# Performance work log

Measured on AMD Instinct MI355X. Metric: run time of the kernel, lower is better.

## Reference

```python
import jax, jax.numpy as jnp
import numpy as np

B, T, F, H = 128, 512, 128, 512
ODE_STEPS = 2
MAX_DT = 1.0


def setup_inputs() -> dict:
    key = jax.random.key(0)
    ks = jax.random.split(key, 8)
    xavier = lambda k, shape: jax.random.uniform(
        k, shape, jnp.float32, -1.0, 1.0) * np.sqrt(6.0 / (shape[0] + shape[1]))
    return {
        "x": jax.random.normal(ks[0], (B, T, F), jnp.float32),
        "time_diffs": jax.random.uniform(ks[1], (B, T), jnp.float32),
        "Wz": xavier(ks[2], (H, F + H)), "bz": jnp.zeros((H,), jnp.float32),
        "Wr": xavier(ks[3], (H, F + H)), "br": jnp.zeros((H,), jnp.float32),
        "Wg": xavier(ks[4], (H, F + H)), "bg": jnp.zeros((H,), jnp.float32),
    }


def reference(x, time_diffs, Wz, bz, Wr, br, Wg, bg):
    hidden = Wz.shape[0]

    def ode_func(x_t, h):
        # dh/dt = (1 - z) * (g - h)
        xh = jnp.concatenate([x_t, h], axis=-1)           # [b, F+H]
        z = jax.nn.sigmoid(xh @ Wz.T + bz)
        r = jax.nn.sigmoid(xh @ Wr.T + br)
        g = jnp.tanh(jnp.concatenate([x_t, r * h], axis=-1) @ Wg.T + bg)
        return (1.0 - z) * (g - h)

    def rk4(x_t, h, dt):
        k1 = ode_func(x_t, h)
        k2 = ode_func(x_t, h + 0.5 * dt * k1)
        k3 = ode_func(x_t, h + 0.5 * dt * k2)
        k4 = ode_func(x_t, h + dt * k3)
        return h + (dt / 6.0) * (k1 + 2.0 * k2 + 2.0 * k3 + k4)

    def step(h, inp):
        x_t, td = inp                                     # [b,F], [b]
        dt = (jnp.minimum(td, MAX_DT) / ODE_STEPS)[:, None]
        for _ in range(ODE_STEPS):                        # small fixed count
            h = rk4(x_t, h, dt)
        return h, h

    h0 = jnp.zeros((x.shape[0], hidden), x.dtype)
    _, out = jax.lax.scan(step, h0, (jnp.swapaxes(x, 0, 1), time_diffs.T))
    return jnp.swapaxes(out, 0, 1)                        # [b, T, H]
```

## Files before the change

### kernel.cpp

```cpp
#include <hip/hip_runtime.h>


namespace {
constexpr int kB = 128, kT = 512, kF = 128, kH = 512, kFH = 640;
constexpr int QZ4 = 0, QR4 = 16384, QG4 = 32768;
constexpr int WXZ4 = 49152, WXR4 = 57344, WXG4 = 65536;
constexpr size_t CS_OFF = (size_t)73728 * 16;
constexpr float HSCL = 100.0f;
}

typedef _Float16 h2_t __attribute__((ext_vector_type(2)));

__device__ __forceinline__ unsigned short f2h(float f) {
  return __builtin_bit_cast(unsigned short, (_Float16)f);
}
__device__ __forceinline__ unsigned pack2h(float a, float b) {
  return (unsigned)f2h(a) | ((unsigned)f2h(b) << 16);
}
__device__ __forceinline__ float dot2(unsigned w, unsigned h, float acc) {
  return __builtin_amdgcn_fdot2(__builtin_bit_cast(h2_t, w),
                                __builtin_bit_cast(h2_t, h), acc, false);
}
__device__ __forceinline__ float dot2x4(uint4 w, uint4 h, float acc) {
  acc = dot2(w.x, h.x, acc); acc = dot2(w.y, h.y, acc);
  acc = dot2(w.z, h.z, acc); acc = dot2(w.w, h.w, acc);
  return acc;
}
__device__ __forceinline__ uint4 pk8(const float* s) {
  const float4 a = *(const float4*)s;
  const float4 b = *(const float4*)(s + 4);
  uint4 o;
  o.x = pack2h(a.x, a.y); o.y = pack2h(a.z, a.w);
  o.z = pack2h(b.x, b.y); o.w = pack2h(b.z, b.w);
  return o;
}
__device__ __forceinline__ int sd4(unsigned a, unsigned b, int acc) {
  return __builtin_amdgcn_sdot4((int)a, (int)b, acc, false);
}
__device__ __forceinline__ void dslice(const uint4 w, const unsigned* hq,
                                       int p, int& acc) {
  acc = sd4(w.x, hq[4 * p + 0], acc);
  acc = sd4(w.y, hq[4 * p + 1], acc);
  acc = sd4(w.z, hq[4 * p + 2], acc);
  acc = sd4(w.w, hq[4 * p + 3], acc);
}

#define DECL_OPQ(v, ptr, s)                                          \
  uint4 v = (ptr)[(s) * kH];                                         \
  asm volatile("" : "+v"(v.x), "+v"(v.y), "+v"(v.z), "+v"(v.w))

__global__ void quant_weights(const float* __restrict__ Wz,
                              const float* __restrict__ Wr,
                              const float* __restrict__ Wg,
                              void* __restrict__ ws) {
  const int bx = blockIdx.x;
  const int gate = bx >> 9, j = bx & 511;
  const float* W = (gate == 0) ? Wz : (gate == 1) ? Wr : Wg;
  const float* row = W + (size_t)j * kFH;
  const int lane = threadIdx.x;
  uint4* ws4 = (uint4*)ws;

  const float* src = row + kF + lane * 8;
  float v[8]; float m = 0.f;
#pragma unroll
  for (int i = 0; i < 8; ++i) { v[i] = src[i]; m = fmaxf(m, fabsf(v[i])); }
#pragma unroll
  for (int off = 32; off; off >>= 1) m = fmaxf(m, __shfl_xor(m, off));
  const float inv = 127.f / m;
  unsigned u0 = 0, u1 = 0;
#pragma unroll
  for (int i = 0; i < 4; ++i) {
    int q = __float2int_rn(v[i] * inv); q = max(-127, min(127, q));
    u0 |= ((unsigned)(q & 255)) << (8 * i);
  }
#pragma unroll
  for (int i = 0; i < 4; ++i) {
    int q = __float2int_rn(v[4 + i] * inv); q = max(-127, min(127, q));
    u1 |= ((unsigned)(q & 255)) << (8 * i);
  }
  const int p = lane >> 1, sub = lane & 1;
  const int qbase = (gate == 0) ? QZ4 : (gate == 1) ? QR4 : QG4;
  *(uint2*)((char*)ws + ((size_t)(qbase + p * kH + j)) * 16 + sub * 8) =
      make_uint2(u0, u1);
  if (lane < 16) {
    const int xbase = (gate == 0) ? WXZ4 : (gate == 1) ? WXR4 : WXG4;
    ws4[xbase + lane * kH + j] = pk8(row + lane * 8);
  }
  if (lane == 0)
    ((float*)((char*)ws + CS_OFF))[gate * 512 + j] = m / (127.f * HSCL);
}

__global__ __launch_bounds__(1024, 4) void cgru_i8s(
    const float* __restrict__ x, const float* __restrict__ td,
    const float* __restrict__ bz, const float* __restrict__ br,
    const float* __restrict__ bg, const uint4* __restrict__ ws,
    float* __restrict__ out) {
  __shared__ uint4 WLa[2][6][kH];
  __shared__ uint4 WLg[2][3][kH];
  __shared__ unsigned hq[kH / 4];
  __shared__ unsigned rq[kH / 4];
  __shared__ unsigned xpk[kF / 2];
  __shared__ float gpart[kH];

  const int b = blockIdx.x;
  const int tid = threadIdx.x;
  const int j = tid & (kH - 1);
  const int half = tid >> 9;

  const uint4* __restrict__ wQa = ws + (half ? QR4 : QZ4) + j;
  const uint4* __restrict__ wQg = ws + QG4 + j;
  const uint4* __restrict__ wxa = ws + (half ? WXR4 : WXZ4) + j;
  const uint4* __restrict__ wxg = ws + WXG4 + j;
  const float* cs = (const float*)((const char*)ws + CS_OFF);
  const float csa = cs[(half ? 512 : 0) + j];
  const float csg = cs[1024 + j];

  DECL_OPQ(a0, wQa, 0); DECL_OPQ(a1, wQa, 1); DECL_OPQ(a2, wQa, 2);
  DECL_OPQ(a3, wQa, 3); DECL_OPQ(a4, wQa, 4); DECL_OPQ(a5, wQa, 5);
  DECL_OPQ(a6, wQa, 6); DECL_OPQ(a7, wQa, 7);
  {
    const uint4* qa = ws + (half ? QR4 : QZ4);
#pragma unroll
    for (int q = 0; q < 6; ++q) WLa[half][q][j] = qa[(8 + q) * kH + j];
#pragma unroll
    for (int q = 0; q < 3; ++q)
      WLg[half][q][j] = (ws + QG4)[((half ? 16 : 0) + q) * kH + j];
  }

  const float ba = half ? br[j] : bz[j];
  const float bgv = bg[j];
  float hb = 0.f, hs = 0.f, kacc = 0.f, zv = 0.f, dtv = 0.f;
  if (tid < kH / 4) hq[tid] = 0;

  for (int t = 0; t < kT; ++t) {
    if (tid < kF / 2) {
      const float2 xv =
          *(const float2*)(x + ((size_t)b * kT + t) * kF + 2 * tid);
      xpk[tid] = pack2h(xv.x, xv.y);
    }
    __syncthreads();

    const uint4* xp4 = (const uint4*)xpk;
    float ax = ba;
#pragma unroll 4
    for (int p = 0; p < 16; ++p) ax = dot2x4(wxa[p * kH], xp4[p], ax);
    float agx = half ? 0.f : bgv;
#pragma unroll 4
    for (int p = 0; p < 8; ++p)
      agx = dot2x4(wxg[(half * 8 + p) * kH], xp4[half * 8 + p], agx);
    if (half == 0) dtv = fminf(td[(size_t)b * kT + t], 1.0f) * 0.5f;

    for (int e = 0; e < 8; ++e) {
      const int s = e & 3;
      int ah = 0;
      dslice(a0, hq, 0, ah); dslice(a1, hq, 1, ah);
      dslice(a2, hq, 2, ah); dslice(a3, hq, 3, ah);
      dslice(a4, hq, 4, ah); dslice(a5, hq, 5, ah);
      dslice(a6, hq, 6, ah); dslice(a7, hq, 7, ah);
#pragma unroll
      for (int q = 0; q < 6; ++q)
        dslice(WLa[half][q][j], hq, 8 + q, ah);
#pragma unroll 6
      for (int p = 14; p < 32; ++p)
        dslice(wQa[p * kH], hq, p, ah);
      const float aA = ax + csa * (float)ah;

      if (half == 0) {
        zv = 1.0f / (1.0f + __expf(-aA));
      } else {
        const float r = 1.0f / (1.0f + __expf(-aA));
        const float hv = (float)((const char*)hq)[j] * (1.0f / HSCL);
        int q = __float2int_rn(fminf(fmaxf(r * hv, -1.27f), 1.27f) * HSCL);
        ((char*)rq)[j] = (char)q;
      }
      __syncthreads();

      int gh = 0;
      const int bs = half << 4;
#pragma unroll
      for (int q = 0; q < 3; ++q)
        dslice(WLg[half][q][j], rq, bs + q, gh);
#pragma unroll 4
      for (int p = bs + 3; p < bs + 16; ++p)
        dslice(wQg[p * kH], rq, p, gh);
      const float gp = agx + csg * (float)gh;
      if (half == 1) gpart[j] = gp;
      __syncthreads();

      if (half == 0) {
        const float g = tanhf(gp + gpart[j]);
        const float kk = (1.0f - zv) * (g - hs);
        kacc = (s == 0) ? kk : kacc + ((s == 3) ? 1.0f : 2.0f) * kk;
        float nxt;
        if (s < 3) {
          nxt = fmaf((s == 2 ? 1.0f : 0.5f) * dtv, kk, hb);
        } else {
          hb = fmaf(dtv * (1.0f / 6.0f), kacc, hb);
          nxt = hb;
        }
        hs = nxt;
        int q = __float2int_rn(fminf(fmaxf(nxt, -1.27f), 1.27f) * HSCL);
        ((char*)hq)[j] = (char)q;
      }
      __syncthreads();
    }

    if (half == 0) out[((size_t)b * kT + t) * kH + j] = hb;
  }
}

extern "C" void kernel_launch(void* const* d_in, const int* in_sizes, int n_in,
                              void* d_out, int out_size, void* d_ws, size_t ws_size,
                              hipStream_t stream) {
  const float* x  = (const float*)d_in[0];
  const float* td = (const float*)d_in[1];
  const float* Wz = (const float*)d_in[2];
  const float* bz = (const float*)d_in[3];
  const float* Wr = (const float*)d_in[4];
  const float* br = (const float*)d_in[5];
  const float* Wg = (const float*)d_in[6];
  const float* bg = (const float*)d_in[7];
  float* out = (float*)d_out;

  quant_weights<<<3 * kH, 64, 0, stream>>>(Wz, Wr, Wg, d_ws);
  cgru_i8s<<<kB, 1024, 0, stream>>>(
      x, td, bz, br, bg, (const uint4*)d_ws, out);
}
```

Baseline: 22.36 ms.

## Precompute input-side gate projections for all timesteps in a parallel kernel

Adds a separate kernel that computes the x-dependent parts of the z, r and g pre-activations, including biases, for every (batch, timestep). Results are stored as fp16 in the workspace. The recurrent kernel then loads these values instead of doing the x dot products and the extra barrier inside the serial time loop. The cost is a large workspace buffer (about 200 MB) with its write and read traffic, plus extra fp16 rounding of the input projections. The old path is kept as a fallback when the workspace is too small.

```diff
diff --git a/kernel.cpp b/kernel.cpp
--- a/kernel.cpp
+++ b/kernel.cpp
@@ -6,6 +6,8 @@
 constexpr int QZ4 = 0, QR4 = 16384, QG4 = 32768;
 constexpr int WXZ4 = 49152, WXR4 = 57344, WXG4 = 65536;
 constexpr size_t CS_OFF = (size_t)73728 * 16;
+constexpr size_t AXP_OFF = 1310720;
+constexpr size_t AXP_BYTES = (size_t)kB * kT * 3 * kH * 2;
 constexpr float HSCL = 100.0f;
 }
 
@@ -16,6 +18,9 @@
 }
 __device__ __forceinline__ unsigned pack2h(float a, float b) {
   return (unsigned)f2h(a) | ((unsigned)f2h(b) << 16);
+}
+__device__ __forceinline__ float h2f(unsigned short u) {
+  return (float)__builtin_bit_cast(_Float16, u);
 }
 __device__ __forceinline__ float dot2(unsigned w, unsigned h, float acc) {
   return __builtin_amdgcn_fdot2(__builtin_bit_cast(h2_t, w),
@@ -90,11 +95,49 @@
     ((float*)((char*)ws + CS_OFF))[gate * 512 + j] = m / (127.f * HSCL);
 }
 
+__global__ __launch_bounds__(512) void xpart_pre(
+    const float* __restrict__ x, const float* __restrict__ bz,
+    const float* __restrict__ br, const float* __restrict__ bg,
+    const uint4* __restrict__ ws, unsigned short* __restrict__ axp) {
+  __shared__ unsigned xt[8][64];
+  const int bx = blockIdx.x;
+  const int b = bx >> 6;
+  const int t0 = (bx & 63) * 8;
+  const int tid = threadIdx.x;
+  {
+    const int m = tid >> 6, c = tid & 63;
+    const float2 xv =
+        *(const float2*)(x + ((size_t)b * kT + t0 + m) * kF + 2 * c);
+    xt[m][c] = pack2h(xv.x, xv.y);
+  }
+  __syncthreads();
+#pragma unroll
+  for (int gate = 0; gate < 3; ++gate) {
+    const uint4* wx =
+        ws + ((gate == 0) ? WXZ4 : (gate == 1) ? WXR4 : WXG4) + tid;
+    const float bv = ((gate == 0) ? bz : (gate == 1) ? br : bg)[tid];
+    float acc[8];
+#pragma unroll
+    for (int m = 0; m < 8; ++m) acc[m] = bv;
+#pragma unroll
+    for (int p = 0; p < 16; ++p) {
+      const uint4 w = wx[p * kH];
+#pragma unroll
+      for (int m = 0; m < 8; ++m)
+        acc[m] = dot2x4(w, ((const uint4*)xt[m])[p], acc[m]);
+    }
+#pragma unroll
+    for (int m = 0; m < 8; ++m)
+      axp[(((size_t)b * kT + t0 + m) * 3 + gate) * kH + tid] = f2h(acc[m]);
+  }
+}
+
+template <int XPRE>
 __global__ __launch_bounds__(1024, 4) void cgru_i8s(
     const float* __restrict__ x, const float* __restrict__ td,
     const float* __restrict__ bz, const float* __restrict__ br,
     const float* __restrict__ bg, const uint4* __restrict__ ws,
-    float* __restrict__ out) {
+    const unsigned short* __restrict__ axp, float* __restrict__ out) {
   __shared__ uint4 WLa[2][6][kH];
   __shared__ uint4 WLg[2][3][kH];
   __shared__ unsigned hq[kH / 4];
@@ -131,24 +174,32 @@
   const float bgv = bg[j];
   float hb = 0.f, hs = 0.f, kacc = 0.f, zv = 0.f, dtv = 0.f;
   if (tid < kH / 4) hq[tid] = 0;
+  if constexpr (XPRE) __syncthreads();
 
   for (int t = 0; t < kT; ++t) {
-    if (tid < kF / 2) {
-      const float2 xv =
-          *(const float2*)(x + ((size_t)b * kT + t) * kF + 2 * tid);
-      xpk[tid] = pack2h(xv.x, xv.y);
+    float ax, agx;
+    if constexpr (XPRE) {
+      const size_t bt3 = ((size_t)b * kT + t) * 3;
+      ax = h2f(axp[(bt3 + half) * kH + j]);
+      agx = half ? 0.f : h2f(axp[(bt3 + 2) * kH + j]);
+      if (half == 0) dtv = fminf(td[(size_t)b * kT + t], 1.0f) * 0.5f;
+    } else {
+      if (tid < kF / 2) {
+        const float2 xv =
+            *(const float2*)(x + ((size_t)b * kT + t) * kF + 2 * tid);
+        xpk[tid] = pack2h(xv.x, xv.y);
+      }
+      __syncthreads();
+      const uint4* xp4 = (const uint4*)xpk;
+      ax = ba;
+#pragma unroll 4
+      for (int p = 0; p < 16; ++p) ax = dot2x4(wxa[p * kH], xp4[p], ax);
+      agx = half ? 0.f : bgv;
+#pragma unroll 4
+      for (int p = 0; p < 8; ++p)
+        agx = dot2x4(wxg[(half * 8 + p) * kH], xp4[half * 8 + p], agx);
+      if (half == 0) dtv = fminf(td[(size_t)b * kT + t], 1.0f) * 0.5f;
     }
-    __syncthreads();
-
-    const uint4* xp4 = (const uint4*)xpk;
-    float ax = ba;
-#pragma unroll 4
-    for (int p = 0; p < 16; ++p) ax = dot2x4(wxa[p * kH], xp4[p], ax);
-    float agx = half ? 0.f : bgv;
-#pragma unroll 4
-    for (int p = 0; p < 8; ++p)
-      agx = dot2x4(wxg[(half * 8 + p) * kH], xp4[half * 8 + p], agx);
-    if (half == 0) dtv = fminf(td[(size_t)b * kT + t], 1.0f) * 0.5f;
 
     for (int e = 0; e < 8; ++e) {
       const int s = e & 3;
@@ -223,6 +274,15 @@
   float* out = (float*)d_out;
 
   quant_weights<<<3 * kH, 64, 0, stream>>>(Wz, Wr, Wg, d_ws);
-  cgru_i8s<<<kB, 1024, 0, stream>>>(
-      x, td, bz, br, bg, (const uint4*)d_ws, out);
-}
+
+  unsigned short* axp = (unsigned short*)((char*)d_ws + AXP_OFF);
+  if (ws_size >= AXP_OFF + AXP_BYTES) {
+    xpart_pre<<<kB * (kT / 8), 512, 0, stream>>>(
+        x, bz, br, bg, (const uint4*)d_ws, axp);
+    cgru_i8s<1><<<kB, 1024, 0, stream>>>(
+        x, td, bz, br, bg, (const uint4*)d_ws, axp, out);
+  } else {
+    cgru_i8s<0><<<kB, 1024, 0, stream>>>(
+        x, td, bz, br, bg, (const uint4*)d_ws, axp, out);
+  }
+}
```

After: 19.36 ms (median of 2 runs). 13.4% less time.
